# Kernel tuning notes

Measured on AMD Instinct MI355X. Metric: run time of the kernel, lower is better.

## Reference

```python
import jax, jax.numpy as jnp
import numpy as np


def _ln(x, w, b, eps=1e-5):
    m = jnp.mean(x, -1, keepdims=True)
    v = jnp.mean((x - m) ** 2, -1, keepdims=True)
    return (x - m) / jnp.sqrt(v + eps) * w + b


def _l2norm(x, axis):
    n = jnp.sqrt(jnp.sum(x * x, axis=axis, keepdims=True))
    return x / jnp.maximum(n, 1e-12)


def _bilinear(img, gx, gy):
    # torch F.grid_sample, bilinear, align_corners=False, padding_mode='zeros'
    # img (B,C,H,W); gx, gy (B,N) in normalized [-1,1] coords -> out (B,C,N)
    B, C, H, W = img.shape
    x = ((gx + 1.0) * W - 1.0) * 0.5
    y = ((gy + 1.0) * H - 1.0) * 0.5
    x0f = jnp.floor(x)
    y0f = jnp.floor(y)
    wx1 = x - x0f
    wy1 = y - y0f
    x0 = x0f.astype(jnp.int32)
    y0 = y0f.astype(jnp.int32)
    imgf = img.reshape(B, C, H * W)

    def gat(xi, yi, wv):
        valid = (xi >= 0) & (xi < W) & (yi >= 0) & (yi < H)
        idx = jnp.clip(yi, 0, H - 1) * W + jnp.clip(xi, 0, W - 1)
        vals = jnp.take_along_axis(imgf, idx[:, None, :], axis=2)  # (B,C,N)
        return vals * (wv * valid)[:, None, :]

    return (gat(x0, y0, (1 - wx1) * (1 - wy1)) + gat(x0 + 1, y0, wx1 * (1 - wy1))
            + gat(x0, y0 + 1, (1 - wx1) * wy1) + gat(x0 + 1, y0 + 1, wx1 * wy1))


def _forward(xyz, g14d, v_feats, ext, intr, offsets,
             gate_w1, gate_b1, gate_w2, gate_b2,
             bn_w1, bn_b1, bn_w2, bn_b2, bn_ln_w, bn_ln_b,
             cw, cw2, hw, ln1_w, ln1_b, gw, gln_w, gln_b, mask):
    B, N, _ = xyz.shape
    BV, C, H, W = v_feats.shape
    V = BV // B
    vf = v_feats.reshape(B, V, C, H, W)
    gelu = lambda t: jax.nn.gelu(t, approximate=False)  # torch nn.GELU default

    # ---- PhysicsGatedProjection ----
    scale = jnp.clip(g14d[:, :, 4:7], 0.01, 10.0)
    opacity = jnp.clip(g14d[:, :, 11:12], 0.0, 1.0)
    gate = jax.nn.sigmoid(gelu(jnp.concatenate([scale, opacity], -1) @ gate_w1 + gate_b1) @ gate_w2 + gate_b2)  # (B,N,1)

    pts_homo = jnp.concatenate([xyz, jnp.ones((B, N, 1), xyz.dtype)], -1)  # (B,N,4)
    sum_f = jnp.zeros((B, N, 32), xyz.dtype)
    sum_m = jnp.zeros((B, N, 1), xyz.dtype)
    for v in range(V):  # small fixed view count
        cam = jnp.einsum('bij,bnj->bni', ext[:, v], pts_homo)      # (B,N,3)
        uvh = jnp.einsum('bij,bnj->bni', intr[:, v], cam)          # (B,N,3)
        depth = jnp.clip(uvh[:, :, 2:3], 1e-6, None)
        uv = uvh[:, :, :2] / depth
        grid = jnp.stack([2.0 * uv[:, :, 0] / (W * 14.0) - 1.0,
                          2.0 * uv[:, :, 1] / (H * 14.0) - 1.0], -1) + offsets  # (B,N,2)
        sampled = _bilinear(vf[:, v], grid[:, :, 0], grid[:, :, 1]).transpose(0, 2, 1)  # (B,N,C)
        h = gelu(sampled @ bn_w1 + bn_b1)
        v32 = _ln(h @ bn_w2 + bn_b2, bn_ln_w, bn_ln_b)             # (B,N,32)
        valid = (depth[:, :, 0] > 0.1) & jnp.all(jnp.abs(grid) <= 1.0, -1) & mask
        vm = valid[:, :, None].astype(xyz.dtype)
        sum_f = sum_f + v32 * gate * vm
        sum_m = sum_m + vm
    fused = sum_f / (sum_m + 1e-6)                                 # (B,N,32)

    # ---- NetVLADLoupe ----
    act = jax.nn.softmax(_ln(fused @ cw, ln1_w, ln1_b), -1)        # (B,N,K)
    act = act * mask[:, :, None].astype(fused.dtype)
    a_sum = jnp.sum(act, 1, keepdims=True)                         # (B,1,K)
    a = a_sum * cw2                                                # (B,D,K)
    vlad = jnp.einsum('bnk,bnd->bdk', act, fused) - a              # (B,D,K)
    vlad = _l2norm(vlad, axis=1)
    vlad = vlad.reshape(B, -1)
    vlad = _l2norm(vlad, axis=1)
    out = vlad @ hw                                                # (B,256)
    gates = jax.nn.sigmoid(_ln(out @ gw, gln_w, gln_b))
    return out * gates


def setup_inputs() -> dict:
    key = jax.random.key(0)
    ks = jax.random.split(key, 16)
    B, N, V, C, H, W = 4, 16384, 6, 384, 32, 32
    d = {}
    d['xyz'] = jax.random.normal(ks[0], (B, N, 3)) * 10.0
    d['g14d'] = jax.random.uniform(ks[1], (B, N, 14))
    d['v_feats'] = jax.random.normal(ks[2], (B * V, C, H, W))
    R = jnp.eye(3)[None, None] + 0.05 * jax.random.normal(ks[3], (B, V, 3, 3))
    t = jnp.concatenate([2.0 * jax.random.normal(ks[4], (B, V, 2, 1)),
                         20.0 + 5.0 * jax.random.uniform(ks[5], (B, V, 1, 1))], axis=2)
    d['ext'] = jnp.concatenate([R, t], -1)                          # (B,V,3,4)
    base_K = jnp.array([[200.0, 0.0, 224.0], [0.0, 200.0, 224.0], [0.0, 0.0, 1.0]])
    d['intr'] = base_K[None, None] + 2.0 * jax.random.normal(ks[6], (B, V, 3, 3)) * jnp.array([[1., 0., 1.], [0., 1., 1.], [0., 0., 0.]])
    d['offsets'] = jnp.zeros((B, N, 2))
    d['mask'] = jnp.ones((B, N), dtype=bool)
    # params
    d['gate_w1'] = jax.random.normal(ks[7], (4, 16)) * 0.5
    d['gate_b1'] = jnp.zeros((16,))
    d['gate_w2'] = jax.random.normal(ks[8], (16, 1)) * 0.25
    d['gate_b2'] = jnp.zeros((1,))
    d['bn_w1'] = jax.random.normal(ks[9], (384, 64)) / np.sqrt(384.0)
    d['bn_b1'] = jnp.zeros((64,))
    d['bn_w2'] = jax.random.normal(ks[10], (64, 32)) / 8.0
    d['bn_b2'] = jnp.zeros((32,))
    d['bn_ln_w'] = jnp.ones((32,))
    d['bn_ln_b'] = jnp.zeros((32,))
    d['cw'] = jax.random.normal(ks[11], (32, 64)) / np.sqrt(32.0)
    d['cw2'] = jax.random.normal(ks[12], (1, 32, 64)) / np.sqrt(32.0)
    d['hw'] = jax.random.normal(ks[13], (32 * 64, 256)) / np.sqrt(32.0)
    d['ln1_w'] = jnp.ones((64,))
    d['ln1_b'] = jnp.zeros((64,))
    d['gw'] = jax.random.normal(ks[14], (256, 256)) / 16.0
    d['gln_w'] = jnp.ones((256,))
    d['gln_b'] = jnp.zeros((256,))
    return d


def reference(xyz, g14d, v_feats, ext, intr, offsets, mask,
              gate_w1, gate_b1, gate_w2, gate_b2,
              bn_w1, bn_b1, bn_w2, bn_b2, bn_ln_w, bn_ln_b,
              cw, cw2, hw, ln1_w, ln1_b, gw, gln_w, gln_b):
    return _forward(xyz, g14d, v_feats, ext, intr, offsets,
                    gate_w1, gate_b1, gate_w2, gate_b2,
                    bn_w1, bn_b1, bn_w2, bn_b2, bn_ln_w, bn_ln_b,
                    cw, cw2, hw, ln1_w, ln1_b, gw, gln_w, gln_b, mask)
```

## Files before the change

### kernel.cpp

```cpp
#include <hip/hip_runtime.h>
#include <hip/hip_bf16.h>
#include <math.h>

#define B_ 4
#define N_ 16384
#define V_ 6
#define C_ 384
#define H_ 32
#define W_ 32
#define HW_ 1024

__device__ __forceinline__ float gelu_f(float x){
  return 0.5f * x * (1.0f + erff(x * 0.70710678118654752440f));
}
__device__ __forceinline__ float sigmoid_f(float x){
  return 1.0f / (1.0f + expf(-x));
}
__device__ __forceinline__ float wsum64(float v){
  #pragma unroll
  for (int m = 1; m < 64; m <<= 1) v += __shfl_xor(v, m);
  return v;
}
__device__ __forceinline__ float wmax64(float v){
  #pragma unroll
  for (int m = 1; m < 64; m <<= 1) v = fmaxf(v, __shfl_xor(v, m));
  return v;
}
__device__ __forceinline__ float wsum32(float v){
  #pragma unroll
  for (int m = 1; m < 32; m <<= 1) v += __shfl_xor(v, m);
  return v;
}

__global__ __launch_bounds__(512) void k0_proj(
    const float* __restrict__ vf, const float* __restrict__ w1,
    float* __restrict__ proj)
{
  const int bv  = blockIdx.x >> 5;
  const int px0 = (blockIdx.x & 31) << 5;
  __shared__ float fs[64][32];
  const int t = threadIdx.x;
  const int j = t & 63;
  const int pg = t >> 6;
  const int sc = t >> 3, sq = t & 7;
  float acc0 = 0.f, acc1 = 0.f, acc2 = 0.f, acc3 = 0.f;

  for (int c0 = 0; c0 < C_; c0 += 64){
    const float4 sv = *(const float4*)&vf[((size_t)bv * C_ + c0 + sc) * HW_
                                          + px0 + sq * 4];
    __syncthreads();
    *(float4*)&fs[sc][sq * 4] = sv;
    __syncthreads();
    for (int c = 0; c < 64; ++c){
      const float w = w1[(c0 + c) * 64 + j];
      const float4 hv = *(const float4*)&fs[c][pg * 4];
      acc0 += hv.x * w;
      acc1 += hv.y * w;
      acc2 += hv.z * w;
      acc3 += hv.w * w;
    }
  }
  const size_t ob = ((size_t)bv * HW_ + px0 + pg * 4) * 64 + j;
  proj[ob]           = acc0;
  proj[ob + 64]      = acc1;
  proj[ob + 128]     = acc2;
  proj[ob + 192]     = acc3;
}

__global__ __launch_bounds__(256) void k1a_records(
    const float* __restrict__ xyz, const float* __restrict__ g14d,
    const float* __restrict__ ext, const float* __restrict__ intr,
    const float* __restrict__ offs, const unsigned char* __restrict__ mask,
    const float* __restrict__ gw1, const float* __restrict__ gb1,
    const float* __restrict__ gw2, const float* __restrict__ gb2,
    uint4* __restrict__ rec, float* __restrict__ gate_g,
    float* __restrict__ summ_g)
{
  const int p = blockIdx.x * 256 + threadIdx.x;
  const int b = p >> 14;

  const float* g = g14d + (size_t)p * 14;
  float in0 = fminf(fmaxf(g[4],  0.01f), 10.f);
  float in1 = fminf(fmaxf(g[5],  0.01f), 10.f);
  float in2 = fminf(fmaxf(g[6],  0.01f), 10.f);
  float in3 = fminf(fmaxf(g[11], 0.0f),  1.f);
  float gacc = gb2[0];
  #pragma unroll
  for (int hh = 0; hh < 16; ++hh){
    float tv = gb1[hh] + in0 * gw1[hh] + in1 * gw1[16 + hh]
             + in2 * gw1[32 + hh] + in3 * gw1[48 + hh];
    gacc += gelu_f(tv) * gw2[hh];
  }
  gate_g[p] = sigmoid_f(gacc);

  const float px = xyz[p * 3], py = xyz[p * 3 + 1], pz = xyz[p * 3 + 2];
  const float offx = offs[p * 2], offy = offs[p * 2 + 1];
  const float mval = mask[p] ? 1.f : 0.f;

  float summ = 0.f;
  #pragma unroll
  for (int v = 0; v < V_; ++v){
    const float* E = ext  + (size_t)(b * V_ + v) * 12;
    const float* I = intr + (size_t)(b * V_ + v) * 9;
    float c0 = E[0]*px + E[1]*py + E[2]*pz + E[3];
    float c1 = E[4]*px + E[5]*py + E[6]*pz + E[7];
    float c2 = E[8]*px + E[9]*py + E[10]*pz + E[11];
    float u0 = I[0]*c0 + I[1]*c1 + I[2]*c2;
    float u1 = I[3]*c0 + I[4]*c1 + I[5]*c2;
    float u2 = I[6]*c0 + I[7]*c1 + I[8]*c2;
    float depth = fmaxf(u2, 1e-6f);
    float gx = 2.0f * (u0 / depth) / (W_ * 14.0f) - 1.0f + offx;
    float gy = 2.0f * (u1 / depth) / (H_ * 14.0f) - 1.0f + offy;
    float fx = ((gx + 1.0f) * W_ - 1.0f) * 0.5f;
    float fy = ((gy + 1.0f) * H_ - 1.0f) * 0.5f;
    fx = fminf(fmaxf(fx, -4.0f), 36.0f);
    fy = fminf(fmaxf(fy, -4.0f), 36.0f);
    float fx0 = floorf(fx), fy0 = floorf(fy);
    float wx = fx - fx0, wy = fy - fy0;
    int x0 = (int)fx0, y0 = (int)fy0;
    unsigned vx0 = (x0 >= 0 && x0 < W_), vx1 = (x0 + 1 >= 0 && x0 + 1 < W_);
    unsigned vy0 = (y0 >= 0 && y0 < H_), vy1 = (y0 + 1 >= 0 && y0 + 1 < H_);
    unsigned vbits = (vx0 & vy0) | ((vx1 & vy0) << 1)
                   | ((vx0 & vy1) << 2) | ((vx1 & vy1) << 3);
    float vm = (depth > 0.1f && fabsf(gx) <= 1.0f && fabsf(gy) <= 1.0f) ? mval : 0.f;
    summ += vm;
    unsigned pk = (unsigned)(x0 + 8) | ((unsigned)(y0 + 8) << 8)
                | (vbits << 16) | ((vm > 0.f ? 1u : 0u) << 20);
    uint4 r;
    r.x = __float_as_uint(wx); r.y = __float_as_uint(wy); r.z = pk; r.w = 0u;
    rec[(size_t)v * (B_ * N_) + p] = r;
  }
  summ_g[p] = summ;
}

__global__ __launch_bounds__(256) void k1b_points(
    const uint4* __restrict__ rec, const float* __restrict__ gate_g,
    const float* __restrict__ summ_g, const unsigned char* __restrict__ mask,
    const float* __restrict__ proj,
    const float* __restrict__ b1, const float* __restrict__ w2,
    const float* __restrict__ b2, const float* __restrict__ lnw,
    const float* __restrict__ lnb, const float* __restrict__ cw,
    const float* __restrict__ ln1w, const float* __restrict__ ln1b,
    float* __restrict__ fused_out, float* __restrict__ act_out)
{
  __shared__ float h_s[4][64];
  __shared__ float fu_s[4][32];
  const int wave = threadIdx.x >> 6, lane = threadIdx.x & 63;
  const int p = (blockIdx.x << 2) + wave;
  const int b = p >> 14;
  const int d = lane & 31, half = lane >> 5;

  float w2c[32];
  #pragma unroll
  for (int j = 0; j < 32; ++j) w2c[j] = w2[(half * 32 + j) * 32 + d];
  const float b1v = b1[lane], b2v = b2[d], lnwv = lnw[d], lnbv = lnb[d];
  const float gate = gate_g[p];
  const float summ = summ_g[p];
  const float mval = mask[p] ? 1.f : 0.f;
  const float* __restrict__ prb = proj + (size_t)b * V_ * HW_ * 64;

  float sum_f = 0.f;
  #pragma unroll
  for (int v = 0; v < V_; ++v){
    const uint4 r = rec[(size_t)v * (B_ * N_) + p];
    const float wx = __uint_as_float(r.x), wy = __uint_as_float(r.y);
    const unsigned pk = r.z;
    const int x0 = (int)(pk & 0xFF) - 8, y0 = (int)((pk >> 8) & 0xFF) - 8;
    const float v00 = (float)((pk >> 16) & 1), v10 = (float)((pk >> 17) & 1);
    const float v01 = (float)((pk >> 18) & 1), v11 = (float)((pk >> 19) & 1);
    const float vmf = (float)((pk >> 20) & 1);
    const int x0c = min(max(x0, 0), W_ - 1), x1c = min(max(x0 + 1, 0), W_ - 1);
    const int y0c = min(max(y0, 0), H_ - 1), y1c = min(max(y0 + 1, 0), H_ - 1);
    const float* pr = prb + (size_t)v * HW_ * 64;
    float s = ((1.f - wx) * (1.f - wy) * v00) * pr[(y0c * W_ + x0c) * 64 + lane];
    s += (wx * (1.f - wy) * v10) * pr[(y0c * W_ + x1c) * 64 + lane];
    s += ((1.f - wx) * wy * v01) * pr[(y1c * W_ + x0c) * 64 + lane];
    s += (wx * wy * v11) * pr[(y1c * W_ + x1c) * 64 + lane];
    const float h = gelu_f(s + b1v);

    h_s[wave][lane] = h;
    asm volatile("" ::: "memory");
    const float4* hp = reinterpret_cast<const float4*>(&h_s[wave][half * 32]);
    float yp = 0.f;
    #pragma unroll
    for (int q = 0; q < 8; ++q){
      const float4 hv = hp[q];
      yp += hv.x * w2c[4 * q + 0];
      yp += hv.y * w2c[4 * q + 1];
      yp += hv.z * w2c[4 * q + 2];
      yp += hv.w * w2c[4 * q + 3];
    }
    float yv = yp + __shfl_xor(yp, 32) + b2v;
    float mean = wsum32(yv) * (1.f / 32.f);
    float dv = yv - mean;
    float var = wsum32(dv * dv) * (1.f / 32.f);
    float v32 = dv * rsqrtf(var + 1e-5f) * lnwv + lnbv;
    sum_f += v32 * gate * vmf;
    asm volatile("" ::: "memory");
  }
  const float fu = sum_f / (summ + 1e-6f);
  if (lane < 32){
    fu_s[wave][lane] = fu;
    fused_out[(size_t)p * 32 + lane] = fu;
  }
  asm volatile("" ::: "memory");

  const float4* fp = reinterpret_cast<const float4*>(&fu_s[wave][0]);
  float z = 0.f;
  #pragma unroll
  for (int q = 0; q < 8; ++q){
    const float4 fv = fp[q];
    z += fv.x * cw[(4 * q + 0) * 64 + lane];
    z += fv.y * cw[(4 * q + 1) * 64 + lane];
    z += fv.z * cw[(4 * q + 2) * 64 + lane];
    z += fv.w * cw[(4 * q + 3) * 64 + lane];
  }
  float mean = wsum64(z) * (1.f / 64.f);
  float dz = z - mean;
  float var = wsum64(dz * dz) * (1.f / 64.f);
  float zl = dz * rsqrtf(var + 1e-5f) * ln1w[lane] + ln1b[lane];
  float mx = wmax64(zl);
  float e = expf(zl - mx);
  float ssum = wsum64(e);
  act_out[(size_t)p * 64 + lane] = (e / ssum) * mval;
}

__global__ __launch_bounds__(256) void k2_vlad(
    const float* __restrict__ fused, const float* __restrict__ act,
    float* __restrict__ vlad_acc, float* __restrict__ asum_acc)
{
  __shared__ float act_s[64][64];
  __shared__ float fu_s[64][32];
  const int b = blockIdx.x >> 6, seg = blockIdx.x & 63;
  const int n0 = seg * 256;
  const int t = threadIdx.x, k = t & 63, dg = t >> 6;
  float vacc[8];
  #pragma unroll
  for (int r = 0; r < 8; ++r) vacc[r] = 0.f;
  float asum = 0.f;

  for (int sc = 0; sc < 4; ++sc){
    int nb = n0 + sc * 64;
    #pragma unroll
    for (int i = 0; i < 16; ++i){
      int idx = t + i * 256;
      act_s[idx >> 6][idx & 63] =
        act[((size_t)((b << 14) + nb + (idx >> 6))) * 64 + (idx & 63)];
    }
    #pragma unroll
    for (int i = 0; i < 8; ++i){
      int idx = t + i * 256;
      fu_s[idx >> 5][idx & 31] =
        fused[((size_t)((b << 14) + nb + (idx >> 5))) * 32 + (idx & 31)];
    }
    __syncthreads();
    for (int i = 0; i < 64; ++i){
      float a = act_s[i][k];
      const float* fr = &fu_s[i][dg * 8];
      #pragma unroll
      for (int r = 0; r < 8; ++r) vacc[r] += a * fr[r];
      if (dg == 0) asum += a;
    }
    __syncthreads();
  }
  #pragma unroll
  for (int r = 0; r < 8; ++r)
    atomicAdd(&vlad_acc[b * 2048 + (dg * 8 + r) * 64 + k], vacc[r]);
  if (dg == 0) atomicAdd(&asum_acc[b * 64 + k], asum);
}

__global__ __launch_bounds__(256) void k3a_norm(
    const float* __restrict__ vlad_acc, const float* __restrict__ asum_acc,
    const float* __restrict__ cw2, float* __restrict__ vs1_g,
    float* __restrict__ ginv_g)
{
  const int b = blockIdx.x, t = threadIdx.x;
  __shared__ float vs[2048];
  __shared__ float denom[64];
  __shared__ float redA[4];
  #pragma unroll
  for (int i = 0; i < 8; ++i){
    int idx = t + i * 256;
    vs[idx] = vlad_acc[b * 2048 + idx]
            - asum_acc[b * 64 + (idx & 63)] * cw2[idx];
  }
  __syncthreads();
  if (t < 64){
    float ss = 0.f;
    #pragma unroll
    for (int dd = 0; dd < 32; ++dd){ float x = vs[dd * 64 + t]; ss += x * x; }
    denom[t] = fmaxf(sqrtf(ss), 1e-12f);
  }
  __syncthreads();
  float ls = 0.f;
  #pragma unroll
  for (int i = 0; i < 8; ++i){
    int idx = t + i * 256;
    float x = vs[idx] / denom[idx & 63];
    vs1_g[b * 2048 + idx] = x;
    ls += x * x;
  }
  ls = wsum64(ls);
  if ((t & 63) == 0) redA[t >> 6] = ls;
  __syncthreads();
  if (t == 0){
    float tot = redA[0] + redA[1] + redA[2] + redA[3];
    ginv_g[b] = 1.0f / fmaxf(sqrtf(tot), 1e-12f);
  }
}

__global__ __launch_bounds__(256) void k3b_hw(
    const float* __restrict__ vs1_g, const float* __restrict__ hw,
    float* __restrict__ out_acc)
{
  const int b = blockIdx.x >> 3, ks = blockIdx.x & 7;
  const int t = threadIdx.x;
  __shared__ float xs[256];
  xs[t] = vs1_g[b * 2048 + ks * 256 + t];
  __syncthreads();
  float acc = 0.f;
  #pragma unroll 4
  for (int i = 0; i < 256; ++i)
    acc += xs[i] * hw[(size_t)(ks * 256 + i) * 256 + t];
  atomicAdd(&out_acc[b * 256 + t], acc);
}

__global__ __launch_bounds__(256) void k3c_gate(
    const float* __restrict__ out_acc, const float* __restrict__ ginv_g,
    const float* __restrict__ gww, const float* __restrict__ glnw,
    const float* __restrict__ glnb, float* __restrict__ outp)
{
  const int b = blockIdx.x, t = threadIdx.x;
  __shared__ float out_s[256];
  __shared__ float redB[4], redC[4];
  const float ginv = ginv_g[b];
  const float o = out_acc[b * 256 + t] * ginv;
  out_s[t] = o;
  __syncthreads();
  float gp = 0.f;
  #pragma unroll 4
  for (int i = 0; i < 256; ++i) gp += out_s[i] * gww[i * 256 + t];
  float s1 = wsum64(gp);
  if ((t & 63) == 0) redB[t >> 6] = s1;
  __syncthreads();
  float mean = (redB[0] + redB[1] + redB[2] + redB[3]) * (1.f / 256.f);
  float dv = gp - mean;
  float s2 = wsum64(dv * dv);
  if ((t & 63) == 0) redC[t >> 6] = s2;
  __syncthreads();
  float var = (redC[0] + redC[1] + redC[2] + redC[3]) * (1.f / 256.f);
  float gt = sigmoid_f(dv * rsqrtf(var + 1e-5f) * glnw[t] + glnb[t]);
  outp[b * 256 + t] = o * gt;
}

extern "C" void kernel_launch(void* const* d_in, const int* in_sizes, int n_in,
                              void* d_out, int out_size, void* d_ws, size_t ws_size,
                              hipStream_t stream)
{
  (void)in_sizes; (void)n_in; (void)out_size; (void)ws_size;
  const float* xyz   = (const float*)d_in[0];
  const float* g14d  = (const float*)d_in[1];
  const float* vf    = (const float*)d_in[2];
  const float* ext   = (const float*)d_in[3];
  const float* intr  = (const float*)d_in[4];
  const float* offs  = (const float*)d_in[5];
  const unsigned char* mask = (const unsigned char*)d_in[6];
  const float* gw1   = (const float*)d_in[7];
  const float* gb1   = (const float*)d_in[8];
  const float* gw2   = (const float*)d_in[9];
  const float* gb2   = (const float*)d_in[10];
  const float* bnw1  = (const float*)d_in[11];
  const float* bnb1  = (const float*)d_in[12];
  const float* bnw2  = (const float*)d_in[13];
  const float* bnb2  = (const float*)d_in[14];
  const float* bnlnw = (const float*)d_in[15];
  const float* bnlnb = (const float*)d_in[16];
  const float* cw    = (const float*)d_in[17];
  const float* cw2   = (const float*)d_in[18];
  const float* hw    = (const float*)d_in[19];
  const float* ln1w  = (const float*)d_in[20];
  const float* ln1b  = (const float*)d_in[21];
  const float* gww   = (const float*)d_in[22];
  const float* glnw  = (const float*)d_in[23];
  const float* glnb  = (const float*)d_in[24];

  char* ws = (char*)d_ws;
  float* vlad_acc = (float*)(ws);
  float* asum_acc = (float*)(ws + 32768);
  float* proj     = (float*)(ws + 33792);
  float* fusedb   = (float*)(ws + 6325248);
  float* actb     = (float*)(ws + 14713856);
  uint4* recb     = (uint4*)(ws + 31491072);
  float* gate_g   = (float*)(ws + 37782528);
  float* summ_g   = (float*)(ws + 38044672);
  float* ginv_g   = (float*)(ws + 31491072);
  float* vs1_g    = (float*)(ws + 31491328);
  float* out_acc  = (float*)(ws + 31524096);

  hipMemsetAsync(d_ws, 0, 33792, stream);
  k0_proj    <<<dim3(768),   dim3(512), 0, stream>>>(vf, bnw1, proj);
  k1a_records<<<dim3(256),   dim3(256), 0, stream>>>(
      xyz, g14d, ext, intr, offs, mask, gw1, gb1, gw2, gb2,
      recb, gate_g, summ_g);
  k1b_points <<<dim3(16384), dim3(256), 0, stream>>>(
      recb, gate_g, summ_g, mask, proj,
      bnb1, bnw2, bnb2, bnlnw, bnlnb, cw, ln1w, ln1b, fusedb, actb);
  k2_vlad    <<<dim3(B_ * 64), dim3(256), 0, stream>>>(fusedb, actb, vlad_acc, asum_acc);
  hipMemsetAsync(ws + 31524096, 0, 4096, stream);
  k3a_norm   <<<dim3(B_),    dim3(256), 0, stream>>>(vlad_acc, asum_acc, cw2,
                                                     vs1_g, ginv_g);
  k3b_hw     <<<dim3(32),    dim3(256), 0, stream>>>(vs1_g, hw, out_acc);
  k3c_gate   <<<dim3(B_),    dim3(256), 0, stream>>>(out_acc, ginv_g, gww,
                                                     glnw, glnb, (float*)d_out);
}
```

Measured before the change: 363.4 us.

## Precompute bilinear weights and indices in records; rewrite projection kernel without LDS

k1a now writes the four masked bilinear weights and four clamped texel indices as separate float4/int4 records, so k1b_points no longer unpacks bitfields, clamps or multiplies weights per lane. This takes redundant per-lane index and weight arithmetic out of the hot gather kernel, at the cost of doubling record storage and read traffic. k0_proj is rewritten so each wave reads 8 pixels directly from global memory for every channel, with no shared-memory staging or syncthreads, and uses 256-thread blocks. The direct reads are broadcast loads that rely on cache and give less reuse than the shared tile.

```diff
diff --git a/kernel.cpp b/kernel.cpp
--- a/kernel.cpp
+++ b/kernel.cpp
@@ -9,6 +9,7 @@
 #define H_ 32
 #define W_ 32
 #define HW_ 1024
+#define BN_ (B_ * N_)
 
 __device__ __forceinline__ float gelu_f(float x){
   return 0.5f * x * (1.0f + erff(x * 0.70710678118654752440f));
@@ -32,39 +33,32 @@
   return v;
 }
 
-__global__ __launch_bounds__(512) void k0_proj(
+__global__ __launch_bounds__(256) void k0_proj(
     const float* __restrict__ vf, const float* __restrict__ w1,
     float* __restrict__ proj)
 {
   const int bv  = blockIdx.x >> 5;
   const int px0 = (blockIdx.x & 31) << 5;
-  __shared__ float fs[64][32];
-  const int t = threadIdx.x;
-  const int j = t & 63;
-  const int pg = t >> 6;
-  const int sc = t >> 3, sq = t & 7;
-  float acc0 = 0.f, acc1 = 0.f, acc2 = 0.f, acc3 = 0.f;
-
-  for (int c0 = 0; c0 < C_; c0 += 64){
-    const float4 sv = *(const float4*)&vf[((size_t)bv * C_ + c0 + sc) * HW_
-                                          + px0 + sq * 4];
-    __syncthreads();
-    *(float4*)&fs[sc][sq * 4] = sv;
-    __syncthreads();
-    for (int c = 0; c < 64; ++c){
-      const float w = w1[(c0 + c) * 64 + j];
-      const float4 hv = *(const float4*)&fs[c][pg * 4];
-      acc0 += hv.x * w;
-      acc1 += hv.y * w;
-      acc2 += hv.z * w;
-      acc3 += hv.w * w;
-    }
-  }
-  const size_t ob = ((size_t)bv * HW_ + px0 + pg * 4) * 64 + j;
-  proj[ob]           = acc0;
-  proj[ob + 64]      = acc1;
-  proj[ob + 128]     = acc2;
-  proj[ob + 192]     = acc3;
+  const int wave = threadIdx.x >> 6, lane = threadIdx.x & 63;
+  const int px = px0 + wave * 8;
+  const float* __restrict__ vr = vf + (size_t)bv * C_ * HW_ + px;
+  float acc[8];
+  #pragma unroll
+  for (int i = 0; i < 8; ++i) acc[i] = 0.f;
+
+  #pragma unroll 4
+  for (int c = 0; c < C_; ++c){
+    const float w = w1[c * 64 + lane];
+    const float4 a = *(const float4*)(vr + (size_t)c * HW_);
+    const float4 b4 = *(const float4*)(vr + (size_t)c * HW_ + 4);
+    acc[0] += a.x * w;  acc[1] += a.y * w;
+    acc[2] += a.z * w;  acc[3] += a.w * w;
+    acc[4] += b4.x * w; acc[5] += b4.y * w;
+    acc[6] += b4.z * w; acc[7] += b4.w * w;
+  }
+  const size_t ob = ((size_t)bv * HW_ + px) * 64 + lane;
+  #pragma unroll
+  for (int i = 0; i < 8; ++i) proj[ob + (size_t)i * 64] = acc[i];
 }
 
 __global__ __launch_bounds__(256) void k1a_records(
@@ -73,8 +67,8 @@
     const float* __restrict__ offs, const unsigned char* __restrict__ mask,
     const float* __restrict__ gw1, const float* __restrict__ gb1,
     const float* __restrict__ gw2, const float* __restrict__ gb2,
-    uint4* __restrict__ rec, float* __restrict__ gate_g,
-    float* __restrict__ summ_g)
+    float4* __restrict__ recW, int4* __restrict__ recI,
+    float* __restrict__ gate_g, float* __restrict__ summ_g)
 {
   const int p = blockIdx.x * 256 + threadIdx.x;
   const int b = p >> 14;
@@ -118,25 +112,34 @@
     float fx0 = floorf(fx), fy0 = floorf(fy);
     float wx = fx - fx0, wy = fy - fy0;
     int x0 = (int)fx0, y0 = (int)fy0;
-    unsigned vx0 = (x0 >= 0 && x0 < W_), vx1 = (x0 + 1 >= 0 && x0 + 1 < W_);
-    unsigned vy0 = (y0 >= 0 && y0 < H_), vy1 = (y0 + 1 >= 0 && y0 + 1 < H_);
-    unsigned vbits = (vx0 & vy0) | ((vx1 & vy0) << 1)
-                   | ((vx0 & vy1) << 2) | ((vx1 & vy1) << 3);
+    float v00 = (float)((x0 >= 0 && x0 < W_) && (y0 >= 0 && y0 < H_));
+    float v10 = (float)((x0 + 1 >= 0 && x0 + 1 < W_) && (y0 >= 0 && y0 < H_));
+    float v01 = (float)((x0 >= 0 && x0 < W_) && (y0 + 1 >= 0 && y0 + 1 < H_));
+    float v11 = (float)((x0 + 1 >= 0 && x0 + 1 < W_) && (y0 + 1 >= 0 && y0 + 1 < H_));
     float vm = (depth > 0.1f && fabsf(gx) <= 1.0f && fabsf(gy) <= 1.0f) ? mval : 0.f;
     summ += vm;
-    unsigned pk = (unsigned)(x0 + 8) | ((unsigned)(y0 + 8) << 8)
-                | (vbits << 16) | ((vm > 0.f ? 1u : 0u) << 20);
-    uint4 r;
-    r.x = __float_as_uint(wx); r.y = __float_as_uint(wy); r.z = pk; r.w = 0u;
-    rec[(size_t)v * (B_ * N_) + p] = r;
+    const int x0c = min(max(x0, 0), W_ - 1), x1c = min(max(x0 + 1, 0), W_ - 1);
+    const int y0c = min(max(y0, 0), H_ - 1), y1c = min(max(y0 + 1, 0), H_ - 1);
+    float4 wv;
+    wv.x = (1.f - wx) * (1.f - wy) * v00;
+    wv.y = wx * (1.f - wy) * v10;
+    wv.z = (1.f - wx) * wy * v01;
+    wv.w = wx * wy * v11;
+    int4 iv;
+    iv.x = (y0c * W_ + x0c) | ((vm > 0.f ? 1 : 0) << 16);
+    iv.y = y0c * W_ + x1c;
+    iv.z = y1c * W_ + x0c;
+    iv.w = y1c * W_ + x1c;
+    recW[(size_t)v * BN_ + p] = wv;
+    recI[(size_t)v * BN_ + p] = iv;
   }
   summ_g[p] = summ;
 }
 
 __global__ __launch_bounds__(256) void k1b_points(
-    const uint4* __restrict__ rec, const float* __restrict__ gate_g,
-    const float* __restrict__ summ_g, const unsigned char* __restrict__ mask,
-    const float* __restrict__ proj,
+    const float4* __restrict__ recW, const int4* __restrict__ recI,
+    const float* __restrict__ gate_g, const float* __restrict__ summ_g,
+    const unsigned char* __restrict__ mask, const float* __restrict__ proj,
     const float* __restrict__ b1, const float* __restrict__ w2,
     const float* __restrict__ b2, const float* __restrict__ lnw,
     const float* __restrict__ lnb, const float* __restrict__ cw,
@@ -157,25 +160,19 @@
   const float gate = gate_g[p];
   const float summ = summ_g[p];
   const float mval = mask[p] ? 1.f : 0.f;
-  const float* __restrict__ prb = proj + (size_t)b * V_ * HW_ * 64;
+  const unsigned vbase = (unsigned)(b * V_) * (HW_ * 64) + (unsigned)lane;
 
   float sum_f = 0.f;
   #pragma unroll
   for (int v = 0; v < V_; ++v){
-    const uint4 r = rec[(size_t)v * (B_ * N_) + p];
-    const float wx = __uint_as_float(r.x), wy = __uint_as_float(r.y);
-    const unsigned pk = r.z;
-    const int x0 = (int)(pk & 0xFF) - 8, y0 = (int)((pk >> 8) & 0xFF) - 8;
-    const float v00 = (float)((pk >> 16) & 1), v10 = (float)((pk >> 17) & 1);
-    const float v01 = (float)((pk >> 18) & 1), v11 = (float)((pk >> 19) & 1);
-    const float vmf = (float)((pk >> 20) & 1);
-    const int x0c = min(max(x0, 0), W_ - 1), x1c = min(max(x0 + 1, 0), W_ - 1);
-    const int y0c = min(max(y0, 0), H_ - 1), y1c = min(max(y0 + 1, 0), H_ - 1);
-    const float* pr = prb + (size_t)v * HW_ * 64;
-    float s = ((1.f - wx) * (1.f - wy) * v00) * pr[(y0c * W_ + x0c) * 64 + lane];
-    s += (wx * (1.f - wy) * v10) * pr[(y0c * W_ + x1c) * 64 + lane];
-    s += ((1.f - wx) * wy * v01) * pr[(y1c * W_ + x0c) * 64 + lane];
-    s += (wx * wy * v11) * pr[(y1c * W_ + x1c) * 64 + lane];
+    const float4 wv = recW[(size_t)v * BN_ + p];
+    const int4  iv = recI[(size_t)v * BN_ + p];
+    const float vmf = (float)(iv.x >> 16);
+    const unsigned vb = vbase + (unsigned)(v * HW_ * 64);
+    float s = wv.x * proj[vb + ((unsigned)(iv.x & 0xFFFF) << 6)];
+    s      += wv.y * proj[vb + ((unsigned)iv.y << 6)];
+    s      += wv.z * proj[vb + ((unsigned)iv.z << 6)];
+    s      += wv.w * proj[vb + ((unsigned)iv.w << 6)];
     const float h = gelu_f(s + b1v);
 
     h_s[wave][lane] = h;
@@ -390,20 +387,21 @@
   float* proj     = (float*)(ws + 33792);
   float* fusedb   = (float*)(ws + 6325248);
   float* actb     = (float*)(ws + 14713856);
-  uint4* recb     = (uint4*)(ws + 31491072);
+  float4* recW    = (float4*)(ws + 31491072);
   float* gate_g   = (float*)(ws + 37782528);
   float* summ_g   = (float*)(ws + 38044672);
+  int4*  recI     = (int4*)(ws + 38306816);
   float* ginv_g   = (float*)(ws + 31491072);
   float* vs1_g    = (float*)(ws + 31491328);
   float* out_acc  = (float*)(ws + 31524096);
 
   hipMemsetAsync(d_ws, 0, 33792, stream);
-  k0_proj    <<<dim3(768),   dim3(512), 0, stream>>>(vf, bnw1, proj);
+  k0_proj    <<<dim3(768),   dim3(256), 0, stream>>>(vf, bnw1, proj);
   k1a_records<<<dim3(256),   dim3(256), 0, stream>>>(
       xyz, g14d, ext, intr, offs, mask, gw1, gb1, gw2, gb2,
-      recb, gate_g, summ_g);
+      recW, recI, gate_g, summ_g);
   k1b_points <<<dim3(16384), dim3(256), 0, stream>>>(
-      recb, gate_g, summ_g, mask, proj,
+      recW, recI, gate_g, summ_g, mask, proj,
       bnb1, bnw2, bnb2, bnlnw, bnlnb, cw, ln1w, ln1b, fusedb, actb);
   k2_vlad    <<<dim3(B_ * 64), dim3(256), 0, stream>>>(fusedb, actb, vlad_acc, asum_acc);
   hipMemsetAsync(ws + 31524096, 0, 4096, stream);
```

Result: slower. 420.7 us (+15.8%).

## Precompute bilinear weights and indices per view, batch all view gathers before MLP

Applied to the files above, without the earlier changes.

The record producer now stores the four masked bilinear weights and four clamped texel indices as two float4 per point-view, so the consumer no longer decodes bit-packed fields. The point kernel issues all six views' gathers up front into registers, stages all hidden vectors to shared memory at once, then runs the small matmul and layernorm per view. This is meant to expose more memory-level parallelism and cut per-view ALU work. The cost is double the record traffic, a larger workspace with relocated buffers, and more registers.

```diff
diff --git a/kernel.cpp b/kernel.cpp
--- a/kernel.cpp
+++ b/kernel.cpp
@@ -9,6 +9,7 @@
 #define H_ 32
 #define W_ 32
 #define HW_ 1024
+#define BN_ (B_ * N_)
 
 __device__ __forceinline__ float gelu_f(float x){
   return 0.5f * x * (1.0f + erff(x * 0.70710678118654752440f));
@@ -73,7 +74,7 @@
     const float* __restrict__ offs, const unsigned char* __restrict__ mask,
     const float* __restrict__ gw1, const float* __restrict__ gb1,
     const float* __restrict__ gw2, const float* __restrict__ gb2,
-    uint4* __restrict__ rec, float* __restrict__ gate_g,
+    float4* __restrict__ rec2, float* __restrict__ gate_g,
     float* __restrict__ summ_g)
 {
   const int p = blockIdx.x * 256 + threadIdx.x;
@@ -118,23 +119,33 @@
     float fx0 = floorf(fx), fy0 = floorf(fy);
     float wx = fx - fx0, wy = fy - fy0;
     int x0 = (int)fx0, y0 = (int)fy0;
-    unsigned vx0 = (x0 >= 0 && x0 < W_), vx1 = (x0 + 1 >= 0 && x0 + 1 < W_);
-    unsigned vy0 = (y0 >= 0 && y0 < H_), vy1 = (y0 + 1 >= 0 && y0 + 1 < H_);
-    unsigned vbits = (vx0 & vy0) | ((vx1 & vy0) << 1)
-                   | ((vx0 & vy1) << 2) | ((vx1 & vy1) << 3);
+    float v00 = (float)((x0 >= 0 && x0 < W_) && (y0 >= 0 && y0 < H_));
+    float v10 = (float)((x0 + 1 >= 0 && x0 + 1 < W_) && (y0 >= 0 && y0 < H_));
+    float v01 = (float)((x0 >= 0 && x0 < W_) && (y0 + 1 >= 0 && y0 + 1 < H_));
+    float v11 = (float)((x0 + 1 >= 0 && x0 + 1 < W_) && (y0 + 1 >= 0 && y0 + 1 < H_));
     float vm = (depth > 0.1f && fabsf(gx) <= 1.0f && fabsf(gy) <= 1.0f) ? mval : 0.f;
     summ += vm;
-    unsigned pk = (unsigned)(x0 + 8) | ((unsigned)(y0 + 8) << 8)
-                | (vbits << 16) | ((vm > 0.f ? 1u : 0u) << 20);
-    uint4 r;
-    r.x = __float_as_uint(wx); r.y = __float_as_uint(wy); r.z = pk; r.w = 0u;
-    rec[(size_t)v * (B_ * N_) + p] = r;
+    const int x0c = min(max(x0, 0), W_ - 1), x1c = min(max(x0 + 1, 0), W_ - 1);
+    const int y0c = min(max(y0, 0), H_ - 1), y1c = min(max(y0 + 1, 0), H_ - 1);
+    float4 wv;
+    wv.x = (1.f - wx) * (1.f - wy) * v00;
+    wv.y = wx * (1.f - wy) * v10;
+    wv.z = (1.f - wx) * wy * v01;
+    wv.w = wx * wy * v11;
+    int4 iv;
+    iv.x = (y0c * W_ + x0c) | ((vm > 0.f ? 1 : 0) << 16);
+    iv.y = y0c * W_ + x1c;
+    iv.z = y1c * W_ + x0c;
+    iv.w = y1c * W_ + x1c;
+    const size_t ri = 2 * ((size_t)v * BN_ + p);
+    rec2[ri] = wv;
+    rec2[ri + 1] = *(const float4*)&iv;
   }
   summ_g[p] = summ;
 }
 
 __global__ __launch_bounds__(256) void k1b_points(
-    const uint4* __restrict__ rec, const float* __restrict__ gate_g,
+    const float4* __restrict__ rec2, const float* __restrict__ gate_g,
     const float* __restrict__ summ_g, const unsigned char* __restrict__ mask,
     const float* __restrict__ proj,
     const float* __restrict__ b1, const float* __restrict__ w2,
@@ -143,7 +154,7 @@
     const float* __restrict__ ln1w, const float* __restrict__ ln1b,
     float* __restrict__ fused_out, float* __restrict__ act_out)
 {
-  __shared__ float h_s[4][64];
+  __shared__ float h_s[4][V_][64];
   __shared__ float fu_s[4][32];
   const int wave = threadIdx.x >> 6, lane = threadIdx.x & 63;
   const int p = (blockIdx.x << 2) + wave;
@@ -157,46 +168,50 @@
   const float gate = gate_g[p];
   const float summ = summ_g[p];
   const float mval = mask[p] ? 1.f : 0.f;
-  const float* __restrict__ prb = proj + (size_t)b * V_ * HW_ * 64;
-
-  float sum_f = 0.f;
+  const unsigned vbase = (unsigned)(b * V_) * (HW_ * 64) + (unsigned)lane;
+
+  float hv[V_], vmf[V_];
   #pragma unroll
   for (int v = 0; v < V_; ++v){
-    const uint4 r = rec[(size_t)v * (B_ * N_) + p];
-    const float wx = __uint_as_float(r.x), wy = __uint_as_float(r.y);
-    const unsigned pk = r.z;
-    const int x0 = (int)(pk & 0xFF) - 8, y0 = (int)((pk >> 8) & 0xFF) - 8;
-    const float v00 = (float)((pk >> 16) & 1), v10 = (float)((pk >> 17) & 1);
-    const float v01 = (float)((pk >> 18) & 1), v11 = (float)((pk >> 19) & 1);
-    const float vmf = (float)((pk >> 20) & 1);
-    const int x0c = min(max(x0, 0), W_ - 1), x1c = min(max(x0 + 1, 0), W_ - 1);
-    const int y0c = min(max(y0, 0), H_ - 1), y1c = min(max(y0 + 1, 0), H_ - 1);
-    const float* pr = prb + (size_t)v * HW_ * 64;
-    float s = ((1.f - wx) * (1.f - wy) * v00) * pr[(y0c * W_ + x0c) * 64 + lane];
-    s += (wx * (1.f - wy) * v10) * pr[(y0c * W_ + x1c) * 64 + lane];
-    s += ((1.f - wx) * wy * v01) * pr[(y1c * W_ + x0c) * 64 + lane];
-    s += (wx * wy * v11) * pr[(y1c * W_ + x1c) * 64 + lane];
-    const float h = gelu_f(s + b1v);
-
-    h_s[wave][lane] = h;
-    asm volatile("" ::: "memory");
-    const float4* hp = reinterpret_cast<const float4*>(&h_s[wave][half * 32]);
-    float yp = 0.f;
+    const size_t ri = 2 * ((size_t)v * BN_ + p);
+    const float4 wv = rec2[ri];
+    const float4 ivf = rec2[ri + 1];
+    const int4 iv = *(const int4*)&ivf;
+    vmf[v] = (float)(iv.x >> 16);
+    const unsigned vb = vbase + (unsigned)(v * HW_ * 64);
+    float s = wv.x * proj[vb + ((unsigned)(iv.x & 0xFFFF) << 6)];
+    s      += wv.y * proj[vb + ((unsigned)iv.y << 6)];
+    s      += wv.z * proj[vb + ((unsigned)iv.z << 6)];
+    s      += wv.w * proj[vb + ((unsigned)iv.w << 6)];
+    hv[v] = gelu_f(s + b1v);
+  }
+  #pragma unroll
+  for (int v = 0; v < V_; ++v) h_s[wave][v][lane] = hv[v];
+  asm volatile("" ::: "memory");
+  float yp[V_];
+  #pragma unroll
+  for (int v = 0; v < V_; ++v){
+    const float4* hp = reinterpret_cast<const float4*>(&h_s[wave][v][half * 32]);
+    float y = 0.f;
     #pragma unroll
     for (int q = 0; q < 8; ++q){
-      const float4 hv = hp[q];
-      yp += hv.x * w2c[4 * q + 0];
-      yp += hv.y * w2c[4 * q + 1];
-      yp += hv.z * w2c[4 * q + 2];
-      yp += hv.w * w2c[4 * q + 3];
+      const float4 hq = hp[q];
+      y += hq.x * w2c[4 * q + 0];
+      y += hq.y * w2c[4 * q + 1];
+      y += hq.z * w2c[4 * q + 2];
+      y += hq.w * w2c[4 * q + 3];
     }
-    float yv = yp + __shfl_xor(yp, 32) + b2v;
+    yp[v] = y;
+  }
+  float sum_f = 0.f;
+  #pragma unroll
+  for (int v = 0; v < V_; ++v){
+    float yv = yp[v] + __shfl_xor(yp[v], 32) + b2v;
     float mean = wsum32(yv) * (1.f / 32.f);
     float dv = yv - mean;
     float var = wsum32(dv * dv) * (1.f / 32.f);
     float v32 = dv * rsqrtf(var + 1e-5f) * lnwv + lnbv;
-    sum_f += v32 * gate * vmf;
-    asm volatile("" ::: "memory");
+    sum_f += v32 * gate * vmf[v];
   }
   const float fu = sum_f / (summ + 1e-6f);
   if (lane < 32){
@@ -390,9 +405,9 @@
   float* proj     = (float*)(ws + 33792);
   float* fusedb   = (float*)(ws + 6325248);
   float* actb     = (float*)(ws + 14713856);
-  uint4* recb     = (uint4*)(ws + 31491072);
-  float* gate_g   = (float*)(ws + 37782528);
-  float* summ_g   = (float*)(ws + 38044672);
+  float4* rec2    = (float4*)(ws + 31491072);
+  float* gate_g   = (float*)(ws + 44073472);
+  float* summ_g   = (float*)(ws + 44335616);
   float* ginv_g   = (float*)(ws + 31491072);
   float* vs1_g    = (float*)(ws + 31491328);
   float* out_acc  = (float*)(ws + 31524096);
@@ -401,9 +416,9 @@
   k0_proj    <<<dim3(768),   dim3(512), 0, stream>>>(vf, bnw1, proj);
   k1a_records<<<dim3(256),   dim3(256), 0, stream>>>(
       xyz, g14d, ext, intr, offs, mask, gw1, gb1, gw2, gb2,
-      recb, gate_g, summ_g);
+      rec2, gate_g, summ_g);
   k1b_points <<<dim3(16384), dim3(256), 0, stream>>>(
-      recb, gate_g, summ_g, mask, proj,
+      rec2, gate_g, summ_g, mask, proj,
       bnb1, bnw2, bnb2, bnlnw, bnlnb, cw, ln1w, ln1b, fusedb, actb);
   k2_vlad    <<<dim3(B_ * 64), dim3(256), 0, stream>>>(fusedb, actb, vlad_acc, asum_acc);
   hipMemsetAsync(ws + 31524096, 0, 4096, stream);
```

After: 375.0 us. +3.2%, slower.
